# Optimization experiments

Measured on AMD Instinct MI355X. Metric: run time of the kernel, lower is better.

Reference implementation:

```python
import jax, jax.numpy as jnp
import numpy as np

N_DIM = 1024   # nodes (rows of s, rows of Kweight)
IN_DIM = 1024  # nodes / feature dim (cols of s, rows of Qweight, side of Gmat)
H_DIM = 64
B = 16


def setup_inputs() -> dict:
    key = jax.random.key(0)
    k1, k2, k3, k4 = jax.random.split(key, 4)
    s = jax.random.normal(k1, (N_DIM, B, IN_DIM), dtype=jnp.float32)
    Gmat = jax.random.uniform(k2, (IN_DIM, IN_DIM), dtype=jnp.float32)
    # torch init: rand * (4/d)**0.5 - (1/d)**0.5  => U[-(1/d)**0.5, (1/d)**0.5]... kept faithful
    Qweight = jax.random.uniform(k3, (IN_DIM, H_DIM), dtype=jnp.float32) * (4.0 / IN_DIM) ** 0.5 - (1.0 / IN_DIM) ** 0.5
    Kweight = jax.random.uniform(k4, (N_DIM, H_DIM), dtype=jnp.float32) * (4.0 / N_DIM) ** 0.5 - (1.0 / N_DIM) ** 0.5
    return {"s": s, "Gmat": Gmat, "Qweight": Qweight, "Kweight": Kweight}


def reference(s, Gmat, Qweight, Kweight):
    h_dim = Qweight.shape[1]
    inv_sqrt_h = 1.0 / jnp.sqrt(jnp.float32(h_dim))
    # q: einsum('ijk,km->ijm', s, Qw).permute(1,0,2) -> (B, n, h)
    q = jnp.einsum('nbi,ih->bnh', s, Qweight)
    # k: s.permute(1,2,0) einsum Kw then permute(0,2,1) -> (B, h, i)
    k = jnp.einsum('nbi,nh->bhi', s, Kweight)
    # squared (non-softmax) attention scores: (B, n, i)
    att = jnp.square(jnp.einsum('bnh,bhi->bni', q, k) * inv_sqrt_h + 1e-9)
    # adjacency aggregation: (B, n, i) @ (i, i)
    att = jnp.einsum('bni,ij->bnj', att, Gmat)
    # row-normalize and permute back to (n, B, i)
    s_t = jnp.sum(att, axis=2, keepdims=True) + 0.001
    return (att / s_t).transpose(1, 0, 2)
```

## Files before the change

### kernel.cpp

```cpp
#include <hip/hip_runtime.h>
#include <hip/hip_bf16.h>
#include <stdint.h>

typedef unsigned short u16;
typedef unsigned int   u32;

#define N_DIM  1024
#define IN_DIM 1024
#define H_DIM  64
#define BATCH  16

typedef __bf16 bf16x8 __attribute__((ext_vector_type(8)));
typedef float  f32x4  __attribute__((ext_vector_type(4)));

__device__ inline u16 f2bf(float f) {
    union { float f; u32 u; } v; v.f = f;
    u32 u = v.u;
    return (u16)((u + 0x7fffu + ((u >> 16) & 1u)) >> 16);
}
__device__ inline u32 pack2(float a, float b) {
    __hip_bfloat162 h = __float22bfloat162_rn(float2{a, b});
    union { __hip_bfloat162 h; u32 u; } cv; cv.h = h; return cv.u;
}

__device__ inline void gl_lds16(const u16* g, u16* l) {
    __builtin_amdgcn_global_load_lds(
        (const __attribute__((address_space(1))) u32*)g,
        (__attribute__((address_space(3))) u32*)l, 16, 0, 0);
}

__global__ __launch_bounds__(256) void prep(
        const float* __restrict__ G, const float* __restrict__ Q,
        const float* __restrict__ Kw, u16* __restrict__ Gbt,
        float* __restrict__ Grp, u16* __restrict__ QT, u16* __restrict__ KwT) {
    int bid = blockIdx.x;
    if (bid >= 256) {
        int idx = (bid - 256) * 256 + threadIdx.x;
        const float* src = (idx < 65536) ? Q : Kw;
        u16* dst = (idx < 65536) ? QT : KwT;
        int i = idx & 65535;
        int h = i >> 10;
        int n = i & 1023;
        dst[h * 1024 + n] = f2bf(src[n * 64 + h]);
        return;
    }
    __shared__ float tile[64][65];
    int jt = bid & 15, it = bid >> 4;
    int i0 = it * 64, j0 = jt * 64;
    int tx = threadIdx.x & 63, ty = threadIdx.x >> 6;
    for (int r = 0; r < 16; ++r) {
        int i = ty * 16 + r;
        tile[i][tx] = G[(size_t)(i0 + i) * 1024 + j0 + tx];
    }
    __syncthreads();
    for (int r = 0; r < 16; ++r) {
        int j = ty * 16 + r;
        Gbt[(size_t)(j0 + j) * 1024 + i0 + tx] = f2bf(tile[tx][j]);
    }
    if (ty == 0) {
        float sum = 0.f;
        for (int j = 0; j < 64; ++j) sum += tile[tx][j];
        Grp[jt * 1024 + i0 + tx] = sum;
    }
}

__global__ __launch_bounds__(512, 4) void qkt(
        const float* __restrict__ s, const u16* __restrict__ QT,
        const u16* __restrict__ KwT, const float* __restrict__ Grp,
        u16* __restrict__ qws, u16* __restrict__ ktws, float* __restrict__ Grsum) {
    int b = blockIdx.y;
    int t = threadIdx.x, lane = t & 63, w = t >> 6, quad = lane >> 4, l15 = lane & 15;
    __shared__ __align__(16) u16 sh[2][2][64][34];
    float* red = (float*)sh;

    if (blockIdx.z == 0) {
        if (blockIdx.y == 0 && t < 64) {
            int i = blockIdx.x * 64 + t;
            float g = 0.f;
            for (int jt = 0; jt < 16; ++jt) g += Grp[jt * 1024 + i];
            Grsum[i] = g;
        }
        int n0 = blockIdx.x * 64;
        int wm = (w & 3) * 16;
        int kb = (w >> 2) * 512;
        const float* arow = s + (size_t)(n0 + wm + l15) * (BATCH * IN_DIM)
                              + (size_t)b * IN_DIM + kb + quad * 8;
        const u16* bbase = QT + (size_t)l15 * 1024 + kb + quad * 8;

        f32x4 acc[4] = {};
        float4 A0[3], A1[3];
        bf16x8 Bf[2][4];
        A0[0] = ((const float4*)arow)[0];
        A1[0] = ((const float4*)arow)[1];
        A0[1] = ((const float4*)(arow + 32))[0];
        A1[1] = ((const float4*)(arow + 32))[1];
#pragma unroll
        for (int ct = 0; ct < 4; ++ct)
            Bf[0][ct] = *(const bf16x8*)&bbase[ct * 16384];

#pragma unroll
        for (int st = 0; st < 16; ++st) {
            int cur = st % 3, cb = st & 1;
            if (st < 14) {
                const float4* ap = (const float4*)(arow + (size_t)(st + 2) * 32);
                A0[(st + 2) % 3] = ap[0];
                A1[(st + 2) % 3] = ap[1];
            }
            if (st < 15) {
#pragma unroll
                for (int ct = 0; ct < 4; ++ct)
                    Bf[cb ^ 1][ct] = *(const bf16x8*)&bbase[ct * 16384 + (st + 1) * 32];
            }
            float4 fa = A0[cur], fb = A1[cur];
            union { uint4 u; bf16x8 v; } cu;
            cu.u = (uint4){ pack2(fa.x, fa.y), pack2(fa.z, fa.w),
                            pack2(fb.x, fb.y), pack2(fb.z, fb.w) };
#pragma unroll
            for (int ct = 0; ct < 4; ++ct)
                acc[ct] = __builtin_amdgcn_mfma_f32_16x16x32_bf16(cu.v, Bf[cb][ct], acc[ct], 0, 0, 0);
        }

        if (w >= 4) {
            float* dst = red + ((w - 4) * 64 + lane) * 16;
#pragma unroll
            for (int ct = 0; ct < 4; ++ct) *(f32x4*)&dst[ct * 4] = acc[ct];
        }
        __syncthreads();
        if (w < 4) {
            const float* sp2 = red + (w * 64 + lane) * 16;
            u16* ob = qws + (size_t)b * 65536;
#pragma unroll
            for (int ct = 0; ct < 4; ++ct) {
                f32x4 o = *(const f32x4*)&sp2[ct * 4];
#pragma unroll
                for (int r = 0; r < 4; ++r) {
                    int m = n0 + wm + quad * 4 + r;
                    ob[(size_t)m * 64 + ct * 16 + l15] = f2bf(acc[ct][r] + o[r]);
                }
            }
        }
        return;
    }

    int i0 = blockIdx.x * 64;
    int half = w >> 2;
    int wm = (w & 3) * 16;
    int shalf = t >> 8, nr = (t & 255) >> 3, iofs = (t & 7) * 8;
    const float* sp = s + (size_t)(shalf * 512 + nr) * (BATCH * IN_DIM)
                        + (size_t)b * IN_DIM + i0 + iofs;
    const u16* bbase = KwT + (size_t)l15 * 1024 + half * 512 + quad * 8;

    f32x4 acc[4] = {};
    float4 P0[2], P1[2];
    bf16x8 Bf[2][4];
    P0[0] = ((const float4*)sp)[0];
    P1[0] = ((const float4*)sp)[1];
    {
        const float4* p = (const float4*)(sp + (size_t)32 * 16384);
        P0[1] = p[0]; P1[1] = p[1];
    }
#pragma unroll
    for (int ct = 0; ct < 4; ++ct)
        Bf[0][ct] = *(const bf16x8*)&bbase[ct * 16384];

#pragma unroll
    for (int c = 0; c < 16; ++c) {
        int buf = c & 1;
        float4 fa = P0[buf], fb = P1[buf];
        u16* wp = &sh[shalf][buf][iofs][nr];
        wp[0]   = f2bf(fa.x);
        wp[34]  = f2bf(fa.y);
        wp[68]  = f2bf(fa.z);
        wp[102] = f2bf(fa.w);
        wp[136] = f2bf(fb.x);
        wp[170] = f2bf(fb.y);
        wp[204] = f2bf(fb.z);
        wp[238] = f2bf(fb.w);
        __syncthreads();
        if (c < 14) {
            const float4* p = (const float4*)(sp + (size_t)(c + 2) * 32 * 16384);
            P0[buf] = p[0]; P1[buf] = p[1];
        }
        if (c < 15) {
#pragma unroll
            for (int ct = 0; ct < 4; ++ct)
                Bf[(c + 1) & 1][ct] = *(const bf16x8*)&bbase[ct * 16384 + (c + 1) * 32];
        }
        const u32* ap = (const u32*)&sh[half][buf][wm + l15][quad * 8];
        union { u32 u[4]; bf16x8 v; } au;
        au.u[0] = ap[0]; au.u[1] = ap[1]; au.u[2] = ap[2]; au.u[3] = ap[3];
#pragma unroll
        for (int ct = 0; ct < 4; ++ct)
            acc[ct] = __builtin_amdgcn_mfma_f32_16x16x32_bf16(au.v, Bf[buf][ct], acc[ct], 0, 0, 0);
    }

    __syncthreads();
    if (w >= 4) {
        float* dst = red + ((w - 4) * 64 + lane) * 16;
#pragma unroll
        for (int ct = 0; ct < 4; ++ct) *(f32x4*)&dst[ct * 4] = acc[ct];
    }
    __syncthreads();
    if (w < 4) {
        const float* sp2 = red + (w * 64 + lane) * 16;
        u16* ob = ktws + (size_t)b * 65536;
#pragma unroll
        for (int ct = 0; ct < 4; ++ct) {
            f32x4 o = *(const f32x4*)&sp2[ct * 4];
#pragma unroll
            for (int r = 0; r < 4; ++r) {
                int i = i0 + wm + quad * 4 + r;
                ob[(size_t)i * 64 + ct * 16 + l15] = f2bf(acc[ct][r] + o[r]);
            }
        }
    }
}

__global__ __launch_bounds__(256, 2) void gemm_fused(
        const u16* __restrict__ qws, const u16* __restrict__ ktws,
        const u16* __restrict__ Gbt, const float* __restrict__ Grsum,
        float* __restrict__ out) {
    int b = blockIdx.z;
    int n0 = blockIdx.x * 256, m0 = blockIdx.y * 128;
    const u16* qb = qws  + (size_t)b * 65536;
    const u16* kb = ktws + (size_t)b * 65536;
    __shared__ __align__(16) u16 As[2][128 * 40];
    __shared__ __align__(16) u16 Bs[3][256 * 32];
    __shared__ __align__(16) u16 ktc[2][32 * 68];
    __shared__ float rs[128];
    int t = threadIdx.x, lane = t & 63, w = t >> 6, quad = lane >> 4, l15 = lane & 15;
    int ti = w & 1;
    int wm = (w >> 1) * 64;
    int wn = (w & 1) * 128;

    if (t < 128) rs[t] = 0.f;

    bf16x8 qf[4][2];
#pragma unroll
    for (int j = 0; j < 4; ++j)
#pragma unroll
        for (int kick = 0; kick < 2; ++kick)
            qf[j][kick] = *(const bf16x8*)&qb[(size_t)(m0 + wm + j*16 + l15) * 64 + kick*32 + quad*8];

    int br = t >> 2, bc = (t & 3) * 8;
#pragma unroll
    for (int g4 = 0; g4 < 4; ++g4)
        gl_lds16(Gbt + (size_t)(n0 + br + g4*64) * 1024 + bc, &Bs[0][(br + g4*64) * 32 + bc]);
    int ir = t >> 3, ch = (t & 7) * 8;
    {
        uint4 k0 = *(const uint4*)&kb[(size_t)ir * 64 + ch];
        *(uint4*)&ktc[0][ir * 68 + ch] = k0;
    }

    f32x4 acc[4][8] = {};
    float partial[4] = {0.f, 0.f, 0.f, 0.f};

    for (int kk = 0; kk <= 32; ++kk) {
        int sb = kk & 1;
        __syncthreads();
        if (kk < 31) {
            int dst = (kk + 1) % 3;
#pragma unroll
            for (int g4 = 0; g4 < 4; ++g4)
                gl_lds16(Gbt + (size_t)(n0 + br + g4*64) * 1024 + (kk+1)*32 + bc,
                         &Bs[dst][(br + g4*64) * 32 + bc]);
        }
        uint4 kregn;
        if (kk < 31)
            kregn = *(const uint4*)&kb[(size_t)((kk + 1) * 32 + ir) * 64 + ch];
        if (kk < 32) {
            f32x4 sacc[4] = {};
#pragma unroll
            for (int kick = 0; kick < 2; ++kick) {
                bf16x8 ktf = *(const bf16x8*)&ktc[sb][(ti*16 + l15) * 68 + kick*32 + quad*8];
#pragma unroll
                for (int j = 0; j < 4; ++j)
                    sacc[j] = __builtin_amdgcn_mfma_f32_16x16x32_bf16(ktf, qf[j][kick], sacc[j], 0, 0, 0);
            }
            float4 g = *(const float4*)&Grsum[kk * 32 + ti * 16 + quad * 4];
#pragma unroll
            for (int j = 0; j < 4; ++j) {
                float v0 = sacc[j][0] * 0.125f + 1e-9f; v0 *= v0;
                float v1 = sacc[j][1] * 0.125f + 1e-9f; v1 *= v1;
                float v2 = sacc[j][2] * 0.125f + 1e-9f; v2 *= v2;
                float v3 = sacc[j][3] * 0.125f + 1e-9f; v3 *= v3;
                partial[j] += v0 * g.x + v1 * g.y + v2 * g.z + v3 * g.w;
                uint2 pk = { pack2(v0, v1), pack2(v2, v3) };
                *(uint2*)&As[sb][(wm + j*16 + l15) * 40 + ti*16 + quad*4] = pk;
            }
        }
        if (kk > 0) {
            int bb = (kk - 1) % 3;
            int kh = quad * 8;
            bf16x8 af[4];
#pragma unroll
            for (int i = 0; i < 4; ++i)
                af[i] = *(const bf16x8*)&As[sb ^ 1][(wm + i*16 + l15) * 40 + kh];
#pragma unroll
            for (int jh = 0; jh < 2; ++jh) {
                bf16x8 bfr[4];
#pragma unroll
                for (int j = 0; j < 4; ++j)
                    bfr[j] = *(const bf16x8*)&Bs[bb][(wn + jh*64 + j*16 + l15) * 32 + kh];
#pragma unroll
                for (int i = 0; i < 4; ++i)
#pragma unroll
                    for (int j = 0; j < 4; ++j)
                        acc[i][jh*4 + j] = __builtin_amdgcn_mfma_f32_16x16x32_bf16(af[i], bfr[j], acc[i][jh*4 + j], 0, 0, 0);
            }
        }
        if (kk < 31)
            *(uint4*)&ktc[sb ^ 1][ir * 68 + ch] = kregn;
    }

#pragma unroll
    for (int j = 0; j < 4; ++j) {
        partial[j] += __shfl_xor(partial[j], 16, 64);
        partial[j] += __shfl_xor(partial[j], 32, 64);
    }
    if (quad == 0)
#pragma unroll
        for (int j = 0; j < 4; ++j) atomicAdd(&rs[wm + j*16 + l15], partial[j]);
    __syncthreads();
    if (t < 128) rs[t] = 1.0f / (rs[t] + 0.001f);
    __syncthreads();

#pragma unroll
    for (int i = 0; i < 4; ++i) {
        float4 rv = *(const float4*)&rs[wm + i * 16 + quad * 4];
        float rva[4] = { rv.x, rv.y, rv.z, rv.w };
#pragma unroll
        for (int r = 0; r < 4; ++r) {
            int m = m0 + wm + i * 16 + quad * 4 + r;
            float* orow = out + (size_t)m * (BATCH * IN_DIM) + (size_t)b * IN_DIM + n0 + wn;
#pragma unroll
            for (int j = 0; j < 8; ++j)
                orow[j * 16 + l15] = acc[i][j][r] * rva[r];
        }
    }
}

extern "C" void kernel_launch(void* const* d_in, const int* in_sizes, int n_in,
                              void* d_out, int out_size, void* d_ws, size_t ws_size,
                              hipStream_t stream) {
    const float* s  = (const float*)d_in[0];
    const float* G  = (const float*)d_in[1];
    const float* Q  = (const float*)d_in[2];
    const float* Kw = (const float*)d_in[3];
    float* out = (float*)d_out;
    char* ws = (char*)d_ws;

    u16*   qws   = (u16*)(ws);
    u16*   ktws  = (u16*)(ws + (size_t)(2u << 20));
    u16*   Gbt   = (u16*)(ws + (size_t)(4u << 20));
    u16*   QT    = (u16*)(ws + (size_t)(6u << 20));
    u16*   KwT   = (u16*)(ws + (size_t)(6u << 20) + (128u << 10));
    float* Grsum = (float*)(ws + (size_t)(6u << 20) + (256u << 10));
    float* Grp   = (float*)(ws + (size_t)(6u << 20) + (260u << 10));

    prep<<<768, 256, 0, stream>>>(G, Q, Kw, Gbt, Grp, QT, KwT);
    qkt<<<dim3(16, 16, 2), 512, 0, stream>>>(s, QT, KwT, Grp, qws, ktws, Grsum);
    gemm_fused<<<dim3(4, 8, 16), 256, 0, stream>>>(qws, ktws, Gbt, Grsum, out);
}
```

Baseline: 192.7 us.

## Warp-specialize fused GEMM into score-producer and G-matmul consumer waves

Grows the fused kernel block to 512 threads. Four waves compute the squared attention scores into LDS as producers, and the other four consume them in the Gmat MFMA GEMM, with the Gmat tiles prefetched two stages ahead into a 4-deep buffer. Grsum is staged in LDS and the ktc row pitch is padded to 72. The aim is to overlap the score MFMAs and epilogue with the main GEMM instead of serializing them in one wave set. It adds LDS use and more barriers, and may reduce occupancy.

```diff
diff --git a/kernel.cpp b/kernel.cpp
--- a/kernel.cpp
+++ b/kernel.cpp
@@ -216,7 +216,7 @@
     }
 }
 
-__global__ __launch_bounds__(256, 2) void gemm_fused(
+__global__ __launch_bounds__(512, 2) void gemm_fused(
         const u16* __restrict__ qws, const u16* __restrict__ ktws,
         const u16* __restrict__ Gbt, const float* __restrict__ Grsum,
         float* __restrict__ out) {
@@ -225,117 +225,135 @@
     const u16* qb = qws  + (size_t)b * 65536;
     const u16* kb = ktws + (size_t)b * 65536;
     __shared__ __align__(16) u16 As[2][128 * 40];
-    __shared__ __align__(16) u16 Bs[3][256 * 32];
-    __shared__ __align__(16) u16 ktc[2][32 * 68];
+    __shared__ __align__(16) u16 Bs[4][256 * 32];
+    __shared__ __align__(16) u16 ktc[2][32 * 72];
+    __shared__ __align__(16) float Grs[1024];
     __shared__ float rs[128];
     int t = threadIdx.x, lane = t & 63, w = t >> 6, quad = lane >> 4, l15 = lane & 15;
-    int ti = w & 1;
-    int wm = (w >> 1) * 64;
-    int wn = (w & 1) * 128;
-
-    if (t < 128) rs[t] = 0.f;
-
-    bf16x8 qf[4][2];
-#pragma unroll
-    for (int j = 0; j < 4; ++j)
-#pragma unroll
-        for (int kick = 0; kick < 2; ++kick)
-            qf[j][kick] = *(const bf16x8*)&qb[(size_t)(m0 + wm + j*16 + l15) * 64 + kick*32 + quad*8];
-
-    int br = t >> 2, bc = (t & 3) * 8;
-#pragma unroll
-    for (int g4 = 0; g4 < 4; ++g4)
-        gl_lds16(Gbt + (size_t)(n0 + br + g4*64) * 1024 + bc, &Bs[0][(br + g4*64) * 32 + bc]);
-    int ir = t >> 3, ch = (t & 7) * 8;
-    {
-        uint4 k0 = *(const uint4*)&kb[(size_t)ir * 64 + ch];
-        *(uint4*)&ktc[0][ir * 68 + ch] = k0;
-    }
-
-    f32x4 acc[4][8] = {};
-    float partial[4] = {0.f, 0.f, 0.f, 0.f};
-
-    for (int kk = 0; kk <= 32; ++kk) {
-        int sb = kk & 1;
-        __syncthreads();
-        if (kk < 31) {
-            int dst = (kk + 1) % 3;
+
+    if (w < 4) {
+        int ti = w & 1;
+        int wm = (w >> 1) * 64;
+        ((float4*)Grs)[t] = ((const float4*)Grsum)[t];
+        if (t < 128) rs[t] = 0.f;
+
+        bf16x8 qf[4][2];
+#pragma unroll
+        for (int j = 0; j < 4; ++j)
+#pragma unroll
+            for (int kick = 0; kick < 2; ++kick)
+                qf[j][kick] = *(const bf16x8*)&qb[(size_t)(m0 + wm + j*16 + l15) * 64 + kick*32 + quad*8];
+
+        int ir = t >> 3, ch = (t & 7) * 8;
+        {
+            uint4 k0 = *(const uint4*)&kb[(size_t)ir * 64 + ch];
+            *(uint4*)&ktc[0][ir * 72 + ch] = k0;
+        }
+        float partial[4] = {0.f, 0.f, 0.f, 0.f};
+        __syncthreads();
+
+        for (int kk = 0; kk <= 32; ++kk) {
+            if (kk < 32) {
+                int sb = kk & 1;
+                f32x4 sacc[4] = {};
+#pragma unroll
+                for (int kick = 0; kick < 2; ++kick) {
+                    bf16x8 ktf = *(const bf16x8*)&ktc[sb][(ti*16 + l15) * 72 + kick*32 + quad*8];
+#pragma unroll
+                    for (int j = 0; j < 4; ++j)
+                        sacc[j] = __builtin_amdgcn_mfma_f32_16x16x32_bf16(ktf, qf[j][kick], sacc[j], 0, 0, 0);
+                }
+                uint4 kregn;
+                if (kk < 31)
+                    kregn = *(const uint4*)&kb[(size_t)((kk + 1) * 32 + ir) * 64 + ch];
+                float4 g = *(const float4*)&Grs[kk * 32 + ti * 16 + quad * 4];
+#pragma unroll
+                for (int j = 0; j < 4; ++j) {
+                    float v0 = sacc[j][0] * 0.125f + 1e-9f; v0 *= v0;
+                    float v1 = sacc[j][1] * 0.125f + 1e-9f; v1 *= v1;
+                    float v2 = sacc[j][2] * 0.125f + 1e-9f; v2 *= v2;
+                    float v3 = sacc[j][3] * 0.125f + 1e-9f; v3 *= v3;
+                    partial[j] += v0 * g.x + v1 * g.y + v2 * g.z + v3 * g.w;
+                    uint2 pk = { pack2(v0, v1), pack2(v2, v3) };
+                    *(uint2*)&As[sb][(wm + j*16 + l15) * 40 + ti*16 + quad*4] = pk;
+                }
+                if (kk < 31)
+                    *(uint4*)&ktc[sb ^ 1][ir * 72 + ch] = kregn;
+            }
+            __syncthreads();
+        }
+
+#pragma unroll
+        for (int j = 0; j < 4; ++j) {
+            partial[j] += __shfl_xor(partial[j], 16, 64);
+            partial[j] += __shfl_xor(partial[j], 32, 64);
+        }
+        if (quad == 0)
+#pragma unroll
+            for (int j = 0; j < 4; ++j) atomicAdd(&rs[wm + j*16 + l15], partial[j]);
+        __syncthreads();
+        if (t < 128) rs[t] = 1.0f / (rs[t] + 0.001f);
+        __syncthreads();
+    } else {
+        int wc = w - 4;
+        int wm = (wc >> 1) * 64;
+        int wn = (wc & 1) * 128;
+        int ts = t & 255, br = ts >> 2, bc = (ts & 3) * 8;
+#pragma unroll
+        for (int c0 = 0; c0 < 2; ++c0)
 #pragma unroll
             for (int g4 = 0; g4 < 4; ++g4)
-                gl_lds16(Gbt + (size_t)(n0 + br + g4*64) * 1024 + (kk+1)*32 + bc,
-                         &Bs[dst][(br + g4*64) * 32 + bc]);
-        }
-        uint4 kregn;
-        if (kk < 31)
-            kregn = *(const uint4*)&kb[(size_t)((kk + 1) * 32 + ir) * 64 + ch];
-        if (kk < 32) {
-            f32x4 sacc[4] = {};
-#pragma unroll
-            for (int kick = 0; kick < 2; ++kick) {
-                bf16x8 ktf = *(const bf16x8*)&ktc[sb][(ti*16 + l15) * 68 + kick*32 + quad*8];
-#pragma unroll
-                for (int j = 0; j < 4; ++j)
-                    sacc[j] = __builtin_amdgcn_mfma_f32_16x16x32_bf16(ktf, qf[j][kick], sacc[j], 0, 0, 0);
-            }
-            float4 g = *(const float4*)&Grsum[kk * 32 + ti * 16 + quad * 4];
-#pragma unroll
-            for (int j = 0; j < 4; ++j) {
-                float v0 = sacc[j][0] * 0.125f + 1e-9f; v0 *= v0;
-                float v1 = sacc[j][1] * 0.125f + 1e-9f; v1 *= v1;
-                float v2 = sacc[j][2] * 0.125f + 1e-9f; v2 *= v2;
-                float v3 = sacc[j][3] * 0.125f + 1e-9f; v3 *= v3;
-                partial[j] += v0 * g.x + v1 * g.y + v2 * g.z + v3 * g.w;
-                uint2 pk = { pack2(v0, v1), pack2(v2, v3) };
-                *(uint2*)&As[sb][(wm + j*16 + l15) * 40 + ti*16 + quad*4] = pk;
-            }
-        }
-        if (kk > 0) {
-            int bb = (kk - 1) % 3;
-            int kh = quad * 8;
-            bf16x8 af[4];
-#pragma unroll
-            for (int i = 0; i < 4; ++i)
-                af[i] = *(const bf16x8*)&As[sb ^ 1][(wm + i*16 + l15) * 40 + kh];
-#pragma unroll
-            for (int jh = 0; jh < 2; ++jh) {
-                bf16x8 bfr[4];
-#pragma unroll
-                for (int j = 0; j < 4; ++j)
-                    bfr[j] = *(const bf16x8*)&Bs[bb][(wn + jh*64 + j*16 + l15) * 32 + kh];
+                gl_lds16(Gbt + (size_t)(n0 + br + g4*64) * 1024 + c0*32 + bc,
+                         &Bs[c0][(br + g4*64) * 32 + bc]);
+        f32x4 acc[4][8] = {};
+        __syncthreads();
+
+        for (int kk = 0; kk <= 32; ++kk) {
+            if (kk > 0) {
+                int ab = (kk - 1) & 1, bb = (kk - 1) & 3;
+                int kh = quad * 8;
+                bf16x8 af[4];
 #pragma unroll
                 for (int i = 0; i < 4; ++i)
+                    af[i] = *(const bf16x8*)&As[ab][(wm + i*16 + l15) * 40 + kh];
+#pragma unroll
+                for (int jh = 0; jh < 2; ++jh) {
+                    bf16x8 bfr[4];
 #pragma unroll
                     for (int j = 0; j < 4; ++j)
-                        acc[i][jh*4 + j] = __builtin_amdgcn_mfma_f32_16x16x32_bf16(af[i], bfr[j], acc[i][jh*4 + j], 0, 0, 0);
-            }
-        }
-        if (kk < 31)
-            *(uint4*)&ktc[sb ^ 1][ir * 68 + ch] = kregn;
-    }
-
-#pragma unroll
-    for (int j = 0; j < 4; ++j) {
-        partial[j] += __shfl_xor(partial[j], 16, 64);
-        partial[j] += __shfl_xor(partial[j], 32, 64);
-    }
-    if (quad == 0)
-#pragma unroll
-        for (int j = 0; j < 4; ++j) atomicAdd(&rs[wm + j*16 + l15], partial[j]);
-    __syncthreads();
-    if (t < 128) rs[t] = 1.0f / (rs[t] + 0.001f);
-    __syncthreads();
-
-#pragma unroll
-    for (int i = 0; i < 4; ++i) {
-        float4 rv = *(const float4*)&rs[wm + i * 16 + quad * 4];
-        float rva[4] = { rv.x, rv.y, rv.z, rv.w };
-#pragma unroll
-        for (int r = 0; r < 4; ++r) {
-            int m = m0 + wm + i * 16 + quad * 4 + r;
-            float* orow = out + (size_t)m * (BATCH * IN_DIM) + (size_t)b * IN_DIM + n0 + wn;
-#pragma unroll
-            for (int j = 0; j < 8; ++j)
-                orow[j * 16 + l15] = acc[i][j][r] * rva[r];
+                        bfr[j] = *(const bf16x8*)&Bs[bb][(wn + jh*64 + j*16 + l15) * 32 + kh];
+#pragma unroll
+                    for (int i = 0; i < 4; ++i)
+#pragma unroll
+                        for (int j = 0; j < 4; ++j)
+                            acc[i][jh*4 + j] = __builtin_amdgcn_mfma_f32_16x16x32_bf16(af[i], bfr[j], acc[i][jh*4 + j], 0, 0, 0);
+                }
+            }
+            if (kk < 30) {
+                int dst = (kk + 2) & 3;
+#pragma unroll
+                for (int g4 = 0; g4 < 4; ++g4)
+                    gl_lds16(Gbt + (size_t)(n0 + br + g4*64) * 1024 + (kk+2)*32 + bc,
+                             &Bs[dst][(br + g4*64) * 32 + bc]);
+            }
+            __syncthreads();
+        }
+
+        __syncthreads();
+        __syncthreads();
+
+#pragma unroll
+        for (int i = 0; i < 4; ++i) {
+            float4 rv = *(const float4*)&rs[wm + i * 16 + quad * 4];
+            float rva[4] = { rv.x, rv.y, rv.z, rv.w };
+#pragma unroll
+            for (int r = 0; r < 4; ++r) {
+                int m = m0 + wm + i * 16 + quad * 4 + r;
+                float* orow = out + (size_t)m * (BATCH * IN_DIM) + (size_t)b * IN_DIM + n0 + wn;
+#pragma unroll
+                for (int j = 0; j < 8; ++j)
+                    orow[j * 16 + l15] = acc[i][j][r] * rva[r];
+            }
         }
     }
 }
@@ -360,5 +378,5 @@
 
     prep<<<768, 256, 0, stream>>>(G, Q, Kw, Gbt, Grp, QT, KwT);
     qkt<<<dim3(16, 16, 2), 512, 0, stream>>>(s, QT, KwT, Grp, qws, ktws, Grsum);
-    gemm_fused<<<dim3(4, 8, 16), 256, 0, stream>>>(qws, ktws, Gbt, Grsum, out);
-}
+    gemm_fused<<<dim3(4, 8, 16), 512, 0, stream>>>(qws, ktws, Gbt, Grsum, out);
+}
```

Measured after the change: 211.8 us. 1.1x slower.
